# Kernel optimization log

Hardware: AMD Instinct MI355X
Metric: run time of the kernel (lower is better)

The kernel has to match this reference:

```python
import jax, jax.numpy as jnp
import numpy as np

D_MODEL = 1024
NUM_HEADS = 16
D_K = D_MODEL // NUM_HEADS
SCALE = D_K ** -0.5
NEG = -1e9


def setup_inputs() -> dict:
    key = jax.random.key(0)
    ks = jax.random.split(key, 10)
    B, S = 4, 2048
    x = jax.random.normal(ks[0], (B, S, D_MODEL), dtype=jnp.float32)
    # causal mask: True = masked position (upper triangle)
    mask = jnp.broadcast_to(jnp.triu(jnp.ones((S, S), dtype=bool), k=1), (B, S, S))
    init = 1.0 / np.sqrt(D_MODEL)
    def lin(kw, kb):
        W = jax.random.uniform(kw, (D_MODEL, D_MODEL), jnp.float32, -init, init)
        b = jax.random.uniform(kb, (D_MODEL,), jnp.float32, -init, init)
        return W, b
    Wq, bq = lin(ks[1], ks[2])
    Wk, bk = lin(ks[3], ks[4])
    Wv, bv = lin(ks[5], ks[6])
    Wo, bo = lin(ks[7], ks[8])
    return {"x": x, "mask": mask, "Wq": Wq, "bq": bq, "Wk": Wk, "bk": bk,
            "Wv": Wv, "bv": bv, "Wo": Wo, "bo": bo}


def reference(x, mask, Wq, bq, Wk, bk, Wv, bv, Wo, bo):
    B, S, _ = x.shape
    # projections; weights stored as [in, out] (torch Linear applies x @ W.T; here W already transposed)
    def split_heads(t):
        return t.reshape(B, S, NUM_HEADS, D_K).transpose(0, 2, 1, 3)  # [B,H,S,d_k]
    q = split_heads(x @ Wq + bq)
    k = split_heads(x @ Wk + bk)
    v = split_heads(x @ Wv + bv)
    scores = jnp.einsum('bhqd,bhkd->bhqk', q, k) * SCALE  # [B,H,S,S]
    scores = jnp.where(mask[:, None, :, :], NEG, scores)
    attn = jax.nn.softmax(scores, axis=-1)
    # dropout is identity in eval mode
    out = jnp.einsum('bhqk,bhkd->bhqd', attn, v)
    out = out.transpose(0, 2, 1, 3).reshape(B, S, D_MODEL)
    return out @ Wo + bo
```

## Files before the change

kernel.cpp:

```cpp
#include <hip/hip_runtime.h>
#include <hip/hip_bf16.h>

#define D_MODEL 1024
#define NUM_HEADS 16
#define D_K 64
#define S_LEN 2048
#define BATCH 4

typedef unsigned short u16;
typedef __attribute__((ext_vector_type(8))) short bf16x8;
typedef __attribute__((ext_vector_type(4))) float f32x4;

#define MFMA16 __builtin_amdgcn_mfma_f32_16x16x32_bf16

#define Q_SCALE 0.18033688011112042f

__device__ __forceinline__ float bf2f(u16 u) {
    union { unsigned int i; float f; } v; v.i = ((unsigned int)u) << 16; return v.f;
}
__device__ __forceinline__ u16 f2bf(float f) {
    union { unsigned int i; float f; } v; v.f = f;
    unsigned int x = v.i;
    return (u16)((x + 0x7FFFu + ((x >> 16) & 1u)) >> 16);
}

__device__ __forceinline__ void gload16(const u16* g, u16* l) {
    __builtin_amdgcn_global_load_lds(
        (const __attribute__((address_space(1))) unsigned int*)g,
        (__attribute__((address_space(3))) unsigned int*)l, 16, 0, 0);
}

__global__ __launch_bounds__(256) void convert_x(
    const float* __restrict__ x, u16* __restrict__ xb)
{
    const size_t i = ((size_t)blockIdx.x * 256 + threadIdx.x) * 8;
    float4 a = *reinterpret_cast<const float4*>(x + i);
    float4 b = *reinterpret_cast<const float4*>(x + i + 4);
    bf16x8 o;
    o[0] = (short)f2bf(a.x); o[1] = (short)f2bf(a.y);
    o[2] = (short)f2bf(a.z); o[3] = (short)f2bf(a.w);
    o[4] = (short)f2bf(b.x); o[5] = (short)f2bf(b.y);
    o[6] = (short)f2bf(b.z); o[7] = (short)f2bf(b.w);
    *reinterpret_cast<bf16x8*>(xb + i) = o;
}

__global__ __launch_bounds__(256) void transpose_w(
    const float* __restrict__ W0, const float* __restrict__ W1,
    const float* __restrict__ W2, const float* __restrict__ W3,
    u16* __restrict__ T0, u16* __restrict__ T1,
    u16* __restrict__ T2, u16* __restrict__ T3)
{
    const float* W; u16* T;
    switch (blockIdx.z & 3) {
        case 0:  W = W0; T = T0; break;
        case 1:  W = W1; T = T1; break;
        case 2:  W = W2; T = T2; break;
        default: W = W3; T = T3; break;
    }
    __shared__ u16 S[64][72];
    const int tid = threadIdx.x;
    const int k0 = blockIdx.y * 64, n0 = blockIdx.x * 64;

    const int k = tid >> 2, nb = (tid & 3) * 16;
    #pragma unroll
    for (int c = 0; c < 4; ++c) {
        float4 v = *reinterpret_cast<const float4*>(
            W + (size_t)(k0 + k) * D_MODEL + n0 + nb + c * 4);
        S[nb + c * 4 + 0][k] = f2bf(v.x);
        S[nb + c * 4 + 1][k] = f2bf(v.y);
        S[nb + c * 4 + 2][k] = f2bf(v.z);
        S[nb + c * 4 + 3][k] = f2bf(v.w);
    }
    __syncthreads();
    const int n = tid >> 2, kb = (tid & 3) * 16;
    #pragma unroll
    for (int c = 0; c < 2; ++c) {
        bf16x8 o;
        #pragma unroll
        for (int e = 0; e < 8; ++e) o[e] = (short)S[n][kb + c * 8 + e];
        *reinterpret_cast<bf16x8*>(T + (size_t)(n0 + n) * D_MODEL + k0 + kb + c * 8) = o;
    }
}

template <typename TC>
__device__ __forceinline__ void gemm_body(
    const u16* __restrict__ A, const u16* __restrict__ BT,
    const float* __restrict__ bias, TC* __restrict__ C,
    u16* Al, u16* Bl, float oscale)
{
    const int tid = threadIdx.x;
    const int w = tid >> 6, lane = tid & 63;
    const int g = lane >> 4, c16 = lane & 15;
    const int wr = w >> 1, wc = w & 1;
    const int m0 = blockIdx.y * 128, n0 = blockIdx.x * 128;

    int rS[4], uS[4];
    #pragma unroll
    for (int i = 0; i < 4; ++i) {
        const int p = i * 256 + tid;
        rS[i] = p >> 3;
        uS[i] = ((p & 7) ^ (rS[i] & 7)) * 8;
    }

    f32x4 acc[4][4];
    #pragma unroll
    for (int mi = 0; mi < 4; ++mi)
        #pragma unroll
        for (int ni = 0; ni < 4; ++ni) acc[mi][ni] = (f32x4){0.f, 0.f, 0.f, 0.f};

    for (int k0 = 0; k0 < D_MODEL; k0 += 64) {
        #pragma unroll
        for (int i = 0; i < 4; ++i) {
            gload16(A + (size_t)(m0 + rS[i]) * D_MODEL + k0 + uS[i],
                    Al + (size_t)(i * 256 + w * 64) * 8);
            gload16(BT + (size_t)(n0 + rS[i]) * D_MODEL + k0 + uS[i],
                    Bl + (size_t)(i * 256 + w * 64) * 8);
        }
        __syncthreads();

        #pragma unroll
        for (int s = 0; s < 2; ++s) {
            bf16x8 af[4], bfr[4];
            #pragma unroll
            for (int mi = 0; mi < 4; ++mi) {
                const int r = wr * 64 + mi * 16 + c16;
                af[mi] = *reinterpret_cast<const bf16x8*>(
                    &Al[((r << 3) + ((s * 4 + g) ^ (r & 7))) * 8]);
            }
            #pragma unroll
            for (int ni = 0; ni < 4; ++ni) {
                const int r = wc * 64 + ni * 16 + c16;
                bfr[ni] = *reinterpret_cast<const bf16x8*>(
                    &Bl[((r << 3) + ((s * 4 + g) ^ (r & 7))) * 8]);
            }
            #pragma unroll
            for (int mi = 0; mi < 4; ++mi)
                #pragma unroll
                for (int ni = 0; ni < 4; ++ni)
                    acc[mi][ni] = MFMA16(af[mi], bfr[ni], acc[mi][ni], 0, 0, 0);
        }
        __syncthreads();
    }

    float bc[4];
    #pragma unroll
    for (int ni = 0; ni < 4; ++ni) bc[ni] = bias[n0 + wc * 64 + ni * 16 + c16];

    #pragma unroll
    for (int mi = 0; mi < 4; ++mi) {
        #pragma unroll
        for (int ni = 0; ni < 4; ++ni) {
            const int col = n0 + wc * 64 + ni * 16 + c16;
            #pragma unroll
            for (int r = 0; r < 4; ++r) {
                const int row = m0 + wr * 64 + mi * 16 + g * 4 + r;
                const float v = (acc[mi][ni][r] + bc[ni]) * oscale;
                if constexpr (sizeof(TC) == 4) {
                    C[(size_t)row * D_MODEL + col] = v;
                } else {
                    C[(size_t)row * D_MODEL + col] = f2bf(v);
                }
            }
        }
    }
}

__global__ __launch_bounds__(256) void gemm_qkv(
    const u16* __restrict__ A,
    const u16* __restrict__ BTq, const u16* __restrict__ BTk, const u16* __restrict__ BTv,
    const float* __restrict__ bq, const float* __restrict__ bk, const float* __restrict__ bv,
    u16* __restrict__ Cq, u16* __restrict__ Ck, u16* __restrict__ Cv)
{
    __shared__ u16 Al[128 * 64];
    __shared__ u16 Bl[128 * 64];
    const u16* BT; const float* bias; u16* C; float sc;
    switch (blockIdx.z) {
        case 0:  BT = BTq; bias = bq; C = Cq; sc = Q_SCALE; break;
        case 1:  BT = BTk; bias = bk; C = Ck; sc = 1.f; break;
        default: BT = BTv; bias = bv; C = Cv; sc = 1.f; break;
    }
    gemm_body<u16>(A, BT, bias, C, Al, Bl, sc);
}

__global__ __launch_bounds__(256) void gemm_out(
    const u16* __restrict__ A, const u16* __restrict__ BT,
    const float* __restrict__ bias, float* __restrict__ C)
{
    __shared__ u16 Al[128 * 64];
    __shared__ u16 Bl[128 * 64];
    gemm_body<float>(A, BT, bias, C, Al, Bl, 1.f);
}

__global__ __launch_bounds__(256) void transpose_v(
    const u16* __restrict__ Vb, u16* __restrict__ VT)
{
    __shared__ u16 T[64 * 65];
    const int i  = blockIdx.x;
    const int bh = i >> 5, jt = i & 31;
    const int b  = bh >> 4, h = bh & 15;
    const int j0 = jt * 64, hd = h * 64;
    const int tid = threadIdx.x;

    #pragma unroll
    for (int it = 0; it < 2; ++it) {
        int seg = it * 256 + tid;
        int jr = seg >> 3, d0 = (seg & 7) * 8;
        bf16x8 v = *reinterpret_cast<const bf16x8*>(
            Vb + ((size_t)(b * S_LEN + j0 + jr)) * D_MODEL + hd + d0);
        #pragma unroll
        for (int e = 0; e < 8; ++e) T[jr * 65 + d0 + e] = (u16)v[e];
    }
    __syncthreads();
    #pragma unroll
    for (int it = 0; it < 2; ++it) {
        int seg = it * 256 + tid;
        int d = seg >> 3, uj = (seg & 7) * 8;
        bf16x8 o;
        #pragma unroll
        for (int e = 0; e < 8; ++e) o[e] = (short)T[(uj + e) * 65 + d];
        *reinterpret_cast<bf16x8*>(
            VT + ((size_t)bh * 64 + d) * S_LEN + j0 + uj) = o;
    }
}

__global__ __launch_bounds__(256) void flash_attn(
    const u16* __restrict__ Qb, const u16* __restrict__ Kb,
    const u16* __restrict__ VT, u16* __restrict__ AO)
{
    __shared__ u16 K_lds[64 * 64];
    __shared__ u16 V_lds[64 * 64];
    __shared__ u16 P_lds[4 * 16 * 64];

    const int i    = blockIdx.x;
    const int bh   = (i & 7) * 8 + ((i >> 3) >> 4);
    const int pair = (i >> 3) & 15;
    const int b    = bh >> 4, h = bh & 15, hd = h * 64;

    const int tid = threadIdx.x;
    const int w = tid >> 6, lane = tid & 63;
    const int g = lane >> 4, c16 = lane & 15;

    const size_t kbase  = (size_t)b * S_LEN * D_MODEL + hd;
    const size_t vtbase = (size_t)bh * 64 * S_LEN;
    u16* Pw = &P_lds[w * 1024];

    const f32x4 ZERO = {0.f, 0.f, 0.f, 0.f};
    const f32x4 NEGI = {-1e30f, -1e30f, -1e30f, -1e30f};

    int rS[2], uS[2];
    #pragma unroll
    for (int it = 0; it < 2; ++it) {
        const int p = it * 256 + tid;
        rS[it] = p >> 3;
        uS[it] = ((p & 7) ^ (rS[it] & 7)) * 8;
    }

    #pragma unroll
    for (int half = 0; half < 2; ++half) {
        const int qt = half ? (31 - pair) : pair;
        const int q0 = qt * 64 + w * 16;

        const size_t qrow = ((size_t)b * S_LEN + q0 + c16) * D_MODEL + hd;
        const bf16x8 qf0 = *reinterpret_cast<const bf16x8*>(Qb + qrow + g * 8);
        const bf16x8 qf1 = *reinterpret_cast<const bf16x8*>(Qb + qrow + 32 + g * 8);

        f32x4 acc[4];
        #pragma unroll
        for (int dt = 0; dt < 4; ++dt) acc[dt] = ZERO;
        float m = -1e30f, lp = 0.f;

        const int nt = qt + 1;
        for (int jt = 0; jt < nt; ++jt) {
            const int j0 = jt * 64;
            const bool dtile = (jt == qt);

            __syncthreads();
            #pragma unroll
            for (int it = 0; it < 2; ++it) {
                const int p = it * 256 + tid;
                gload16(Kb + kbase + (size_t)(j0 + rS[it]) * D_MODEL + uS[it],
                        K_lds + (size_t)p * 8);
                gload16(VT + vtbase + (size_t)rS[it] * S_LEN + j0 + uS[it],
                        V_lds + (size_t)p * 8);
            }
            __syncthreads();

            f32x4 st[4];
            #pragma unroll
            for (int kt = 0; kt < 4; ++kt) {
                if (dtile && kt > w) { st[kt] = NEGI; continue; }
                const int row = kt * 16 + c16;
                const bf16x8 kf0 = *reinterpret_cast<const bf16x8*>(
                    &K_lds[row * 64 + ((g ^ (row & 7)) << 3)]);
                const bf16x8 kf1 = *reinterpret_cast<const bf16x8*>(
                    &K_lds[row * 64 + (((4 + g) ^ (row & 7)) << 3)]);
                f32x4 t = MFMA16(kf0, qf0, ZERO, 0, 0, 0);
                t = MFMA16(kf1, qf1, t, 0, 0, 0);
                if (dtile && kt == w) {
                    #pragma unroll
                    for (int r = 0; r < 4; ++r)
                        if (g * 4 + r > c16) t[r] = -1e30f;
                }
                st[kt] = t;
            }

            float mx = st[0][0];
            #pragma unroll
            for (int kt = 0; kt < 4; ++kt)
                #pragma unroll
                for (int r = 0; r < 4; ++r) mx = fmaxf(mx, st[kt][r]);
            mx = fmaxf(mx, __shfl_xor(mx, 16));
            mx = fmaxf(mx, __shfl_xor(mx, 32));

            if (__any(mx > m + 11.5f)) {
                const float mn = fmaxf(m, mx);
                const float co = __builtin_amdgcn_exp2f(m - mn);
                lp *= co;
                m = mn;
                float cor[4];
                #pragma unroll
                for (int r = 0; r < 4; ++r) cor[r] = __shfl(co, g * 4 + r);
                #pragma unroll
                for (int dt = 0; dt < 4; ++dt)
                    #pragma unroll
                    for (int r = 0; r < 4; ++r) acc[dt][r] *= cor[r];
            }

            float tsum = 0.f;
            #pragma unroll
            for (int kt = 0; kt < 4; ++kt) {
                const float p0 = __builtin_amdgcn_exp2f(st[kt][0] - m);
                const float p1 = __builtin_amdgcn_exp2f(st[kt][1] - m);
                const float p2 = __builtin_amdgcn_exp2f(st[kt][2] - m);
                const float p3 = __builtin_amdgcn_exp2f(st[kt][3] - m);
                tsum += (p0 + p1) + (p2 + p3);
                ushort4 pw;
                pw.x = f2bf(p0); pw.y = f2bf(p1); pw.z = f2bf(p2); pw.w = f2bf(p3);
                const int u = kt * 2 + (g >> 1);
                *reinterpret_cast<ushort4*>(
                    &Pw[c16 * 64 + ((u ^ (c16 & 7)) << 3) + (g & 1) * 4]) = pw;
            }
            lp += tsum;

            #pragma unroll
            for (int c32 = 0; c32 < 2; ++c32) {
                if (dtile && c32 == 1 && w < 2) continue;
                const bf16x8 pf = *reinterpret_cast<const bf16x8*>(
                    &Pw[c16 * 64 + (((c32 * 4 + g) ^ (c16 & 7)) << 3)]);
                #pragma unroll
                for (int dt = 0; dt < 4; ++dt) {
                    const int vrow = dt * 16 + c16;
                    const bf16x8 vf = *reinterpret_cast<const bf16x8*>(
                        &V_lds[vrow * 64 + (((c32 * 4 + g) ^ (vrow & 7)) << 3)]);
                    acc[dt] = MFMA16(pf, vf, acc[dt], 0, 0, 0);
                }
            }
        }

        float lt = lp + __shfl_xor(lp, 16);
        lt += __shfl_xor(lt, 32);
        const float inv = 1.f / lt;
        float invr[4];
        #pragma unroll
        for (int r = 0; r < 4; ++r) invr[r] = __shfl(inv, g * 4 + r);

        #pragma unroll
        for (int dt = 0; dt < 4; ++dt) {
            #pragma unroll
            for (int r = 0; r < 4; ++r) {
                const size_t orow =
                    ((size_t)b * S_LEN + q0 + g * 4 + r) * D_MODEL + hd + dt * 16 + c16;
                AO[orow] = f2bf(acc[dt][r] * invr[r]);
            }
        }
    }
}

extern "C" void kernel_launch(void* const* d_in, const int* in_sizes, int n_in,
                              void* d_out, int out_size, void* d_ws, size_t ws_size,
                              hipStream_t stream) {
    const float* x  = (const float*)d_in[0];
    const float* Wq = (const float*)d_in[2];
    const float* bq = (const float*)d_in[3];
    const float* Wk = (const float*)d_in[4];
    const float* bk = (const float*)d_in[5];
    const float* Wv = (const float*)d_in[6];
    const float* bv = (const float*)d_in[7];
    const float* Wo = (const float*)d_in[8];
    const float* bo = (const float*)d_in[9];
    float* out = (float*)d_out;

    const int M = BATCH * S_LEN;
    const size_t tsz = (size_t)M * D_MODEL;
    const size_t wsz = (size_t)D_MODEL * D_MODEL;

    u16* xb  = (u16*)d_ws;
    u16* Qb  = xb + tsz;
    u16* Kb  = Qb + tsz;
    u16* Vb  = Kb + tsz;
    u16* VT  = Vb + tsz;
    u16* WTq = VT + tsz;
    u16* WTk = WTq + wsz;
    u16* WTv = WTk + wsz;
    u16* WTo = WTv + wsz;
    u16* AO  = Vb;

    convert_x<<<(int)(tsz / (256 * 8)), 256, 0, stream>>>(x, xb);
    transpose_w<<<dim3(16, 16, 4), 256, 0, stream>>>(
        Wq, Wk, Wv, Wo, WTq, WTk, WTv, WTo);

    gemm_qkv<<<dim3(8, 64, 3), 256, 0, stream>>>(
        xb, WTq, WTk, WTv, bq, bk, bv, Qb, Kb, Vb);

    transpose_v<<<2048, 256, 0, stream>>>(Vb, VT);
    flash_attn<<<1024, 256, 0, stream>>>(Qb, Kb, VT, AO);

    gemm_out<<<dim3(8, 64), 256, 0, stream>>>(AO, WTo, bo, out);
}
```

Before: 206.3 us.

## Process both causal q-tiles concurrently in 8-wave blocks sharing K/V tiles

The attention kernel now launches 512-thread blocks. Four waves handle query tile p and four handle tile 31-p at the same time, so the two tiles are no longer processed one after the other. Each K/V tile is loaded into LDS once and used by both groups, which cuts global-to-LDS traffic and barrier rounds roughly in half and gives more waves per block. The short-tile waves sit idle at barriers once their causal range ends, and the larger block may reduce occupancy. The bf16 packing of probabilities also switches to the hardware v_cvt_pk_bf16_f32 instruction instead of manual rounding.

```diff
diff --git a/kernel.cpp b/kernel.cpp
--- a/kernel.cpp
+++ b/kernel.cpp
@@ -22,6 +22,11 @@
     union { unsigned int i; float f; } v; v.f = f;
     unsigned int x = v.i;
     return (u16)((x + 0x7FFFu + ((x >> 16) & 1u)) >> 16);
+}
+__device__ __forceinline__ unsigned int cvtpk(float lo, float hi) {
+    unsigned int r;
+    asm("v_cvt_pk_bf16_f32 %0, %1, %2" : "=v"(r) : "v"(lo), "v"(hi));
+    return r;
 }
 
 __device__ __forceinline__ void gload16(const u16* g, u16* l) {
@@ -223,22 +228,26 @@
     }
 }
 
-__global__ __launch_bounds__(256) void flash_attn(
+__global__ __launch_bounds__(512, 4) void flash_attn(
     const u16* __restrict__ Qb, const u16* __restrict__ Kb,
     const u16* __restrict__ VT, u16* __restrict__ AO)
 {
     __shared__ u16 K_lds[64 * 64];
     __shared__ u16 V_lds[64 * 64];
-    __shared__ u16 P_lds[4 * 16 * 64];
-
-    const int i    = blockIdx.x;
-    const int bh   = (i & 7) * 8 + ((i >> 3) >> 4);
-    const int pair = (i >> 3) & 15;
-    const int b    = bh >> 4, h = bh & 15, hd = h * 64;
+    __shared__ u16 P_lds[8 * 16 * 64];
+
+    const int i  = blockIdx.x;
+    const int bh = (i & 7) * 8 + ((i >> 3) & 7);
+    const int p  = i >> 6;
+    const int b  = bh >> 4, h = bh & 15, hd = h * 64;
 
     const int tid = threadIdx.x;
     const int w = tid >> 6, lane = tid & 63;
+    const int wq = w & 3;
     const int g = lane >> 4, c16 = lane & 15;
+
+    const int qt = (w < 4) ? p : (31 - p);
+    const int q0 = qt * 64 + wq * 16;
 
     const size_t kbase  = (size_t)b * S_LEN * D_MODEL + hd;
     const size_t vtbase = (size_t)bh * 64 * S_LEN;
@@ -247,131 +256,117 @@
     const f32x4 ZERO = {0.f, 0.f, 0.f, 0.f};
     const f32x4 NEGI = {-1e30f, -1e30f, -1e30f, -1e30f};
 
-    int rS[2], uS[2];
-    #pragma unroll
-    for (int it = 0; it < 2; ++it) {
-        const int p = it * 256 + tid;
-        rS[it] = p >> 3;
-        uS[it] = ((p & 7) ^ (rS[it] & 7)) * 8;
-    }
-
-    #pragma unroll
-    for (int half = 0; half < 2; ++half) {
-        const int qt = half ? (31 - pair) : pair;
-        const int q0 = qt * 64 + w * 16;
-
-        const size_t qrow = ((size_t)b * S_LEN + q0 + c16) * D_MODEL + hd;
-        const bf16x8 qf0 = *reinterpret_cast<const bf16x8*>(Qb + qrow + g * 8);
-        const bf16x8 qf1 = *reinterpret_cast<const bf16x8*>(Qb + qrow + 32 + g * 8);
-
-        f32x4 acc[4];
-        #pragma unroll
-        for (int dt = 0; dt < 4; ++dt) acc[dt] = ZERO;
-        float m = -1e30f, lp = 0.f;
-
-        const int nt = qt + 1;
-        for (int jt = 0; jt < nt; ++jt) {
-            const int j0 = jt * 64;
-            const bool dtile = (jt == qt);
-
-            __syncthreads();
-            #pragma unroll
-            for (int it = 0; it < 2; ++it) {
-                const int p = it * 256 + tid;
-                gload16(Kb + kbase + (size_t)(j0 + rS[it]) * D_MODEL + uS[it],
-                        K_lds + (size_t)p * 8);
-                gload16(VT + vtbase + (size_t)rS[it] * S_LEN + j0 + uS[it],
-                        V_lds + (size_t)p * 8);
+    const int rK = tid >> 3;
+    const int uK = ((tid & 7) ^ (rK & 7)) * 8;
+
+    const size_t qrow = ((size_t)b * S_LEN + q0 + c16) * D_MODEL + hd;
+    const bf16x8 qf0 = *reinterpret_cast<const bf16x8*>(Qb + qrow + g * 8);
+    const bf16x8 qf1 = *reinterpret_cast<const bf16x8*>(Qb + qrow + 32 + g * 8);
+
+    f32x4 acc[4];
+    #pragma unroll
+    for (int dt = 0; dt < 4; ++dt) acc[dt] = ZERO;
+    float m = -1e30f, lp = 0.f;
+
+    const int nt = 32 - p;
+    for (int jt = 0; jt < nt; ++jt) {
+        const int j0 = jt * 64;
+
+        __syncthreads();
+        gload16(Kb + kbase + (size_t)(j0 + rK) * D_MODEL + uK, K_lds + (size_t)tid * 8);
+        gload16(VT + vtbase + (size_t)rK * S_LEN + j0 + uK,    V_lds + (size_t)tid * 8);
+        __syncthreads();
+
+        if (jt > qt) continue;
+        const bool dtile = (jt == qt);
+
+        f32x4 st[4];
+        #pragma unroll
+        for (int kt = 0; kt < 4; ++kt) {
+            if (dtile && kt > wq) { st[kt] = NEGI; continue; }
+            const int row = kt * 16 + c16;
+            const bf16x8 kf0 = *reinterpret_cast<const bf16x8*>(
+                &K_lds[row * 64 + ((g ^ (row & 7)) << 3)]);
+            const bf16x8 kf1 = *reinterpret_cast<const bf16x8*>(
+                &K_lds[row * 64 + (((4 + g) ^ (row & 7)) << 3)]);
+            f32x4 t = MFMA16(kf0, qf0, ZERO, 0, 0, 0);
+            t = MFMA16(kf1, qf1, t, 0, 0, 0);
+            if (dtile && kt == wq) {
+                #pragma unroll
+                for (int r = 0; r < 4; ++r)
+                    if (g * 4 + r > c16) t[r] = -1e30f;
             }
-            __syncthreads();
-
-            f32x4 st[4];
-            #pragma unroll
-            for (int kt = 0; kt < 4; ++kt) {
-                if (dtile && kt > w) { st[kt] = NEGI; continue; }
-                const int row = kt * 16 + c16;
-                const bf16x8 kf0 = *reinterpret_cast<const bf16x8*>(
-                    &K_lds[row * 64 + ((g ^ (row & 7)) << 3)]);
-                const bf16x8 kf1 = *reinterpret_cast<const bf16x8*>(
-                    &K_lds[row * 64 + (((4 + g) ^ (row & 7)) << 3)]);
-                f32x4 t = MFMA16(kf0, qf0, ZERO, 0, 0, 0);
-                t = MFMA16(kf1, qf1, t, 0, 0, 0);
-                if (dtile && kt == w) {
-                    #pragma unroll
-                    for (int r = 0; r < 4; ++r)
-                        if (g * 4 + r > c16) t[r] = -1e30f;
-                }
-                st[kt] = t;
+            st[kt] = t;
+        }
+
+        float mx = st[0][0];
+        #pragma unroll
+        for (int kt = 0; kt < 4; ++kt)
+            #pragma unroll
+            for (int r = 0; r < 4; ++r) mx = fmaxf(mx, st[kt][r]);
+        mx = fmaxf(mx, __shfl_xor(mx, 16));
+        mx = fmaxf(mx, __shfl_xor(mx, 32));
+
+        if (__any(mx > m + 11.5f)) {
+            const float mn = fmaxf(m, mx);
+            const float co = __builtin_amdgcn_exp2f(m - mn);
+            lp *= co;
+            m = mn;
+            float cor[4];
+            #pragma unroll
+            for (int r = 0; r < 4; ++r) cor[r] = __shfl(co, g * 4 + r);
+            #pragma unroll
+            for (int dt = 0; dt < 4; ++dt)
+                #pragma unroll
+                for (int r = 0; r < 4; ++r) acc[dt][r] *= cor[r];
+        }
+
+        float tsum = 0.f;
+        #pragma unroll
+        for (int kt = 0; kt < 4; ++kt) {
+            const float p0 = __builtin_amdgcn_exp2f(st[kt][0] - m);
+            const float p1 = __builtin_amdgcn_exp2f(st[kt][1] - m);
+            const float p2 = __builtin_amdgcn_exp2f(st[kt][2] - m);
+            const float p3 = __builtin_amdgcn_exp2f(st[kt][3] - m);
+            tsum += (p0 + p1) + (p2 + p3);
+            uint2 pw;
+            pw.x = cvtpk(p0, p1);
+            pw.y = cvtpk(p2, p3);
+            const int u = kt * 2 + (g >> 1);
+            *reinterpret_cast<uint2*>(
+                &Pw[c16 * 64 + ((u ^ (c16 & 7)) << 3) + (g & 1) * 4]) = pw;
+        }
+        lp += tsum;
+
+        #pragma unroll
+        for (int c32 = 0; c32 < 2; ++c32) {
+            if (dtile && c32 == 1 && wq < 2) continue;
+            const bf16x8 pf = *reinterpret_cast<const bf16x8*>(
+                &Pw[c16 * 64 + (((c32 * 4 + g) ^ (c16 & 7)) << 3)]);
+            #pragma unroll
+            for (int dt = 0; dt < 4; ++dt) {
+                const int vrow = dt * 16 + c16;
+                const bf16x8 vf = *reinterpret_cast<const bf16x8*>(
+                    &V_lds[vrow * 64 + (((c32 * 4 + g) ^ (vrow & 7)) << 3)]);
+                acc[dt] = MFMA16(pf, vf, acc[dt], 0, 0, 0);
             }
-
-            float mx = st[0][0];
-            #pragma unroll
-            for (int kt = 0; kt < 4; ++kt)
-                #pragma unroll
-                for (int r = 0; r < 4; ++r) mx = fmaxf(mx, st[kt][r]);
-            mx = fmaxf(mx, __shfl_xor(mx, 16));
-            mx = fmaxf(mx, __shfl_xor(mx, 32));
-
-            if (__any(mx > m + 11.5f)) {
-                const float mn = fmaxf(m, mx);
-                const float co = __builtin_amdgcn_exp2f(m - mn);
-                lp *= co;
-                m = mn;
-                float cor[4];
-                #pragma unroll
-                for (int r = 0; r < 4; ++r) cor[r] = __shfl(co, g * 4 + r);
-                #pragma unroll
-                for (int dt = 0; dt < 4; ++dt)
-                    #pragma unroll
-                    for (int r = 0; r < 4; ++r) acc[dt][r] *= cor[r];
-            }
-
-            float tsum = 0.f;
-            #pragma unroll
-            for (int kt = 0; kt < 4; ++kt) {
-                const float p0 = __builtin_amdgcn_exp2f(st[kt][0] - m);
-                const float p1 = __builtin_amdgcn_exp2f(st[kt][1] - m);
-                const float p2 = __builtin_amdgcn_exp2f(st[kt][2] - m);
-                const float p3 = __builtin_amdgcn_exp2f(st[kt][3] - m);
-                tsum += (p0 + p1) + (p2 + p3);
-                ushort4 pw;
-                pw.x = f2bf(p0); pw.y = f2bf(p1); pw.z = f2bf(p2); pw.w = f2bf(p3);
-                const int u = kt * 2 + (g >> 1);
-                *reinterpret_cast<ushort4*>(
-                    &Pw[c16 * 64 + ((u ^ (c16 & 7)) << 3) + (g & 1) * 4]) = pw;
-            }
-            lp += tsum;
-
-            #pragma unroll
-            for (int c32 = 0; c32 < 2; ++c32) {
-                if (dtile && c32 == 1 && w < 2) continue;
-                const bf16x8 pf = *reinterpret_cast<const bf16x8*>(
-                    &Pw[c16 * 64 + (((c32 * 4 + g) ^ (c16 & 7)) << 3)]);
-                #pragma unroll
-                for (int dt = 0; dt < 4; ++dt) {
-                    const int vrow = dt * 16 + c16;
-                    const bf16x8 vf = *reinterpret_cast<const bf16x8*>(
-                        &V_lds[vrow * 64 + (((c32 * 4 + g) ^ (vrow & 7)) << 3)]);
-                    acc[dt] = MFMA16(pf, vf, acc[dt], 0, 0, 0);
-                }
-            }
-        }
-
-        float lt = lp + __shfl_xor(lp, 16);
-        lt += __shfl_xor(lt, 32);
-        const float inv = 1.f / lt;
-        float invr[4];
-        #pragma unroll
-        for (int r = 0; r < 4; ++r) invr[r] = __shfl(inv, g * 4 + r);
-
-        #pragma unroll
-        for (int dt = 0; dt < 4; ++dt) {
-            #pragma unroll
-            for (int r = 0; r < 4; ++r) {
-                const size_t orow =
-                    ((size_t)b * S_LEN + q0 + g * 4 + r) * D_MODEL + hd + dt * 16 + c16;
-                AO[orow] = f2bf(acc[dt][r] * invr[r]);
-            }
+        }
+    }
+
+    float lt = lp + __shfl_xor(lp, 16);
+    lt += __shfl_xor(lt, 32);
+    const float inv = 1.f / lt;
+    float invr[4];
+    #pragma unroll
+    for (int r = 0; r < 4; ++r) invr[r] = __shfl(inv, g * 4 + r);
+
+    #pragma unroll
+    for (int dt = 0; dt < 4; ++dt) {
+        #pragma unroll
+        for (int r = 0; r < 4; ++r) {
+            const size_t orow =
+                ((size_t)b * S_LEN + q0 + g * 4 + r) * D_MODEL + hd + dt * 16 + c16;
+            AO[orow] = f2bf(acc[dt][r] * invr[r]);
         }
     }
 }
@@ -413,7 +408,7 @@
         xb, WTq, WTk, WTv, bq, bk, bv, Qb, Kb, Vb);
 
     transpose_v<<<2048, 256, 0, stream>>>(Vb, VT);
-    flash_attn<<<1024, 256, 0, stream>>>(Qb, Kb, VT, AO);
+    flash_attn<<<1024, 512, 0, stream>>>(Qb, Kb, VT, AO);
 
     gemm_out<<<dim3(8, 64), 256, 0, stream>>>(AO, WTo, bo, out);
 }
```

Result: faster. 200.5 us (-2.8%).
